# Performance work log

Measured on AMD Instinct MI355X. Metric: run time of the kernel, lower is better.

Reference implementation:

```python
import jax, jax.numpy as jnp
import numpy as np

D_IN = 1024
D_OUT = 1024
SEQ = 2048
BATCH = 4


def setup_inputs() -> dict:
    key = jax.random.key(0)
    kx, kq, kk, kv = jax.random.split(key, 4)
    x = jax.random.normal(kx, (BATCH, SEQ, D_IN), dtype=jnp.float32)
    s = 1.0 / np.sqrt(D_IN)
    Wq = jax.random.uniform(kq, (D_IN, D_OUT), dtype=jnp.float32, minval=-s, maxval=s)
    Wk = jax.random.uniform(kk, (D_IN, D_OUT), dtype=jnp.float32, minval=-s, maxval=s)
    Wv = jax.random.uniform(kv, (D_IN, D_OUT), dtype=jnp.float32, minval=-s, maxval=s)
    return {"x": x, "Wq": Wq, "Wk": Wk, "Wv": Wv}


def reference(x, Wq, Wk, Wv):
    d_k = Wq.shape[1]
    q = jnp.einsum('bsd,de->bse', x, Wq)
    k = jnp.einsum('bsd,de->bse', x, Wk)
    v = jnp.einsum('bsd,de->bse', x, Wv)
    # [B, S, S] raw scores
    scores = jnp.einsum('bqe,bke->bqk', q, k)
    S = scores.shape[-1]
    causal = jnp.triu(jnp.ones((S, S), dtype=bool), k=1)  # True above diagonal
    scores = jnp.where(causal, -jnp.inf, scores)
    attn = jax.nn.softmax(scores * (d_k ** -0.5), axis=-1)
    # dropout p=0.0 -> identity
    return jnp.einsum('bqk,bke->bqe', attn, v)
```

## Files before the change

kernel.cpp:

```cpp
#include <hip/hip_runtime.h>
#include <hip/hip_bf16.h>

typedef unsigned short u16;
typedef __bf16 bfx8 __attribute__((ext_vector_type(8)));
typedef float fx4 __attribute__((ext_vector_type(4)));

#define SEQ 2048
#define DIM 1024
#define NBATCH 4
#define SCALE 0.03125f
#define NEL ((size_t)NBATCH * SEQ * DIM)

__device__ inline u16 f2bf(float f) {
    __bf16 h = (__bf16)f;
    return __builtin_bit_cast(unsigned short, h);
}

#define GLL(gp, lp) __builtin_amdgcn_global_load_lds( \
    (const __attribute__((address_space(1))) unsigned int*)(gp), \
    (__attribute__((address_space(3))) unsigned int*)(lp), 16, 0, 0)

__global__ __launch_bounds__(256) void prep(
    const float* __restrict__ X,
    const float* __restrict__ Wq, const float* __restrict__ Wk,
    const float* __restrict__ Wv,
    u16* __restrict__ XB, u16* __restrict__ WB, u16* __restrict__ WTv,
    float* __restrict__ Lrow)
{
    __shared__ u16 t[32][33];
    int bid = blockIdx.x;
    int tid = threadIdx.x;
    if (bid < 8192) {
        size_t i = (size_t)bid * 256 + tid;
        float4 v = ((const float4*)X)[i];
        uint2 pk;
        pk.x = (unsigned)f2bf(v.x) | ((unsigned)f2bf(v.y) << 16);
        pk.y = (unsigned)f2bf(v.z) | ((unsigned)f2bf(v.w) << 16);
        ((uint2*)XB)[i] = pk;
    } else if (bid < 10240) {
        int b2 = bid - 8192;
        const float* W = (b2 < 1024) ? Wq : Wk;
        u16* out = WB + (size_t)(b2 >> 10) * 1024 * 1024;
        size_t i = (size_t)(b2 & 1023) * 256 + tid;
        float4 v = ((const float4*)W)[i];
        uint2 pk;
        pk.x = (unsigned)f2bf(v.x) | ((unsigned)f2bf(v.y) << 16);
        pk.y = (unsigned)f2bf(v.z) | ((unsigned)f2bf(v.w) << 16);
        ((uint2*)out)[i] = pk;
    } else if (bid < 11264) {
        int t2 = bid - 10240;
        int n0 = (t2 & 31) * 32, k0 = (t2 >> 5) * 32;
        int tx = tid & 31, ty = tid >> 5;
        #pragma unroll
        for (int i = 0; i < 32; i += 8)
            t[ty + i][tx] = f2bf(Wv[(size_t)(k0 + ty + i) * 1024 + n0 + tx]);
        __syncthreads();
        #pragma unroll
        for (int i = 0; i < 32; i += 8)
            WTv[(size_t)(n0 + ty + i) * 1024 + k0 + tx] = t[tx][ty + i];
    } else {
        int i = (bid - 11264) * 256 + tid;
        Lrow[i] = 0.0f;
    }
}

__global__ __launch_bounds__(256) void gemm_m(
    const u16* __restrict__ WBk, const u16* __restrict__ WBq, u16* __restrict__ MT)
{
    int m0 = blockIdx.y * 128, n0 = blockIdx.x * 128;
    __shared__ __align__(16) u16 As[128 * 32];
    __shared__ __align__(16) u16 Bs[128 * 32];
    int tid = threadIdx.x, lane = tid & 63, w = tid >> 6;
    int wm = w >> 1, wn = w & 1, lo = lane & 15, qd = lane >> 4;
    fx4 acc[4][4] = {};

    int c0 = tid, c1 = tid + 256;
    const u16* a0 = WBk + (size_t)(m0 + (c0 >> 2)) * 1024 + (((c0 & 3) ^ ((c0 >> 2) & 3)) * 8);
    const u16* a1 = WBk + (size_t)(m0 + (c1 >> 2)) * 1024 + (((c1 & 3) ^ ((c1 >> 2) & 3)) * 8);
    const u16* b0 = WBq + (size_t)(n0 + (c0 >> 2)) * 1024 + (((c0 & 3) ^ ((c0 >> 2) & 3)) * 8);
    const u16* b1 = WBq + (size_t)(n0 + (c1 >> 2)) * 1024 + (((c1 & 3) ^ ((c1 >> 2) & 3)) * 8);

    int sw = (qd ^ (lo & 3)) * 8;
    for (int k0 = 0; k0 < 1024; k0 += 32) {
        GLL(a0 + k0, &As[(size_t)c0 * 8]);
        GLL(a1 + k0, &As[(size_t)c1 * 8]);
        GLL(b0 + k0, &Bs[(size_t)c0 * 8]);
        GLL(b1 + k0, &Bs[(size_t)c1 * 8]);
        __syncthreads();
        bfx8 af[4], bf[4];
        #pragma unroll
        for (int i = 0; i < 4; i++)
            af[i] = *(const bfx8*)(&As[(wm * 64 + i * 16 + lo) * 32 + sw]);
        #pragma unroll
        for (int j = 0; j < 4; j++)
            bf[j] = *(const bfx8*)(&Bs[(wn * 64 + j * 16 + lo) * 32 + sw]);
        #pragma unroll
        for (int i = 0; i < 4; i++)
            #pragma unroll
            for (int j = 0; j < 4; j++)
                acc[i][j] = __builtin_amdgcn_mfma_f32_16x16x32_bf16(af[i], bf[j], acc[i][j], 0, 0, 0);
        __syncthreads();
    }
    #pragma unroll
    for (int i = 0; i < 4; i++)
        #pragma unroll
        for (int j = 0; j < 4; j++)
            #pragma unroll
            for (int r = 0; r < 4; r++)
                MT[(size_t)(m0 + wm * 64 + i * 16 + qd * 4 + r) * 1024
                   + n0 + wn * 64 + j * 16 + lo] = f2bf(acc[i][j][r]);
}

__global__ __launch_bounds__(512) void gemm256(
    const u16* __restrict__ XB, const u16* __restrict__ MT,
    const u16* __restrict__ WTv,
    u16* __restrict__ Yo, u16* __restrict__ VTo)
{
    const u16* Bop = (blockIdx.z == 0) ? MT : WTv;
    const int m0 = blockIdx.y * 256, n0 = blockIdx.x * 256;

    __shared__ __align__(16) u16 SM[65536];

    const int tid = threadIdx.x, lane = tid & 63, w = tid >> 6;
    const int wm = w >> 2, wn = w & 3, lo = lane & 15, qd = lane >> 4;
    const int swl = lo & 7;

    fx4 acc[8][4] = {};

    const u16* sA[4]; const u16* sB[4]; int dofs[4];
    #pragma unroll
    for (int p = 0; p < 4; ++p) {
        int n = p * 512 + tid;
        int row = n >> 3;
        int c = (n & 7) ^ (row & 7);
        sA[p] = XB  + (size_t)(m0 + row) * 1024 + c * 8;
        sB[p] = Bop + (size_t)(n0 + row) * 1024 + c * 8;
        dofs[p] = n * 8;
    }

    auto stage = [&](int kt2) {
        const int bb = (kt2 & 1) * 16384;
        #pragma unroll
        for (int p = 0; p < 4; ++p) GLL(sA[p] + kt2 * 64, &SM[bb + dofs[p]]);
        #pragma unroll
        for (int p = 0; p < 4; ++p) GLL(sB[p] + kt2 * 64, &SM[32768 + bb + dofs[p]]);
    };

    stage(0);
    stage(1);
    asm volatile("s_waitcnt vmcnt(8)" ::: "memory");
    __builtin_amdgcn_s_barrier();
    asm volatile("" ::: "memory");

    bfx8 af[4][2], bfA[2][2], bfB[2][2];

    for (int kt = 0; kt < 16; ++kt) {
        const u16* Ab = SM + (kt & 1) * 16384;
        const u16* Bb = SM + 32768 + (kt & 1) * 16384;

        #pragma unroll
        for (int ph = 0; ph < 4; ++ph) {
            const int mh = ph >> 1, nh = ph & 1;
            if (nh == 0) {
                #pragma unroll
                for (int ii = 0; ii < 4; ++ii)
                    #pragma unroll
                    for (int ks = 0; ks < 2; ++ks)
                        af[ii][ks] = *(const bfx8*)(Ab
                            + (wm * 128 + (mh * 4 + ii) * 16 + lo) * 64
                            + ((ks * 4 + qd) ^ swl) * 8);
            }
            if (ph == 0) {
                #pragma unroll
                for (int jn = 0; jn < 2; ++jn)
                    #pragma unroll
                    for (int ks = 0; ks < 2; ++ks)
                        bfA[jn][ks] = *(const bfx8*)(Bb
                            + (wn * 64 + jn * 16 + lo) * 64
                            + ((ks * 4 + qd) ^ swl) * 8);
            }
            if (ph == 1) {
                #pragma unroll
                for (int jn = 0; jn < 2; ++jn)
                    #pragma unroll
                    for (int ks = 0; ks < 2; ++ks)
                        bfB[jn][ks] = *(const bfx8*)(Bb
                            + (wn * 64 + (2 + jn) * 16 + lo) * 64
                            + ((ks * 4 + qd) ^ swl) * 8);
            }
            __builtin_amdgcn_s_barrier();
            asm volatile("s_waitcnt lgkmcnt(0)" ::: "memory");
            __builtin_amdgcn_sched_barrier(0);
            __builtin_amdgcn_s_setprio(1);
            #pragma unroll
            for (int ii = 0; ii < 4; ++ii)
                #pragma unroll
                for (int jn = 0; jn < 2; ++jn)
                    #pragma unroll
                    for (int ks = 0; ks < 2; ++ks) {
                        if (nh == 0)
                            acc[mh * 4 + ii][jn] = __builtin_amdgcn_mfma_f32_16x16x32_bf16(
                                af[ii][ks], bfA[jn][ks], acc[mh * 4 + ii][jn], 0, 0, 0);
                        else
                            acc[mh * 4 + ii][2 + jn] = __builtin_amdgcn_mfma_f32_16x16x32_bf16(
                                af[ii][ks], bfB[jn][ks], acc[mh * 4 + ii][2 + jn], 0, 0, 0);
                    }
            __builtin_amdgcn_s_setprio(0);
            __builtin_amdgcn_s_barrier();
            asm volatile("" ::: "memory");
        }
        if (kt < 14) stage(kt + 2);
        if (kt < 15) {
            if (kt < 14) asm volatile("s_waitcnt vmcnt(8)" ::: "memory");
            else         asm volatile("s_waitcnt vmcnt(0)" ::: "memory");
            __builtin_amdgcn_s_barrier();
            asm volatile("" ::: "memory");
        }
    }

    if (blockIdx.z == 0) {
        #pragma unroll
        for (int i = 0; i < 8; i++)
            #pragma unroll
            for (int j = 0; j < 4; j++)
                #pragma unroll
                for (int r = 0; r < 4; r++) {
                    int row = m0 + wm * 128 + i * 16 + qd * 4 + r;
                    int col = n0 + wn * 64 + j * 16 + lo;
                    Yo[(size_t)row * 1024 + col] = f2bf(acc[i][j][r]);
                }
    } else {
        u16 (*Ct)[258] = (u16(*)[258])SM;
        const int bb = m0 >> 11;
        const int sbase = m0 & 2047;
        #pragma unroll
        for (int half = 0; half < 2; ++half) {
            __syncthreads();
            if (wm == half) {
                #pragma unroll
                for (int i = 0; i < 8; i++)
                    #pragma unroll
                    for (int j = 0; j < 4; j++)
                        #pragma unroll
                        for (int r = 0; r < 4; r++)
                            Ct[i * 16 + qd * 4 + r][wn * 64 + j * 16 + lo] = f2bf(acc[i][j][r]);
            }
            __syncthreads();
            for (int e = tid; e < 16384; e += 512) {
                int d = e >> 6, s2 = (e & 63) * 2;
                unsigned pk = (unsigned)Ct[s2][d] | ((unsigned)Ct[s2 + 1][d] << 16);
                *(unsigned*)&VTo[((size_t)bb * DIM + (n0 + d)) * SEQ
                                 + sbase + half * 128 + s2] = pk;
            }
        }
    }
}

__global__ __launch_bounds__(512) void sgemm_exp(
    const u16* __restrict__ Y, const u16* __restrict__ XB,
    u16* __restrict__ P, float* __restrict__ Lrow)
{
    int b = blockIdx.y;
    int t = blockIdx.x;
    int i = (int)((sqrtf(8.0f * t + 1.0f) - 1.0f) * 0.5f);
    while ((i + 1) * (i + 2) / 2 <= t) i++;
    while (i * (i + 1) / 2 > t) i--;
    int j = t - i * (i + 1) / 2;

    const u16* Yb = Y + (size_t)b * SEQ * DIM;
    const u16* Xb = XB + (size_t)b * SEQ * DIM;
    u16* Pb = P + (size_t)b * SEQ * SEQ;
    float* Lb = Lrow + (size_t)b * SEQ;

    int m0 = i * 128, n0 = j * 128;

    __shared__ __align__(16) u16 As[128 * 64];
    __shared__ __align__(16) u16 Bs[128 * 64];

    int tid = threadIdx.x, lane = tid & 63, w = tid >> 6;
    int wm = w >> 2, wn = w & 3, lo = lane & 15, qd = lane >> 4;

    fx4 acc[4][2] = {};

    int c0 = tid, c1 = tid + 512;
    const u16* a0 = Yb + (size_t)(m0 + (c0 >> 3)) * 1024 + (((c0 & 7) ^ ((c0 >> 3) & 7)) * 8);
    const u16* a1 = Yb + (size_t)(m0 + (c1 >> 3)) * 1024 + (((c1 & 7) ^ ((c1 >> 3) & 7)) * 8);
    const u16* b0 = Xb + (size_t)(n0 + (c0 >> 3)) * 1024 + (((c0 & 7) ^ ((c0 >> 3) & 7)) * 8);
    const u16* b1 = Xb + (size_t)(n0 + (c1 >> 3)) * 1024 + (((c1 & 7) ^ ((c1 >> 3) & 7)) * 8);

    for (int k0 = 0; k0 < 1024; k0 += 64) {
        GLL(a0 + k0, &As[(size_t)c0 * 8]);
        GLL(a1 + k0, &As[(size_t)c1 * 8]);
        GLL(b0 + k0, &Bs[(size_t)c0 * 8]);
        GLL(b1 + k0, &Bs[(size_t)c1 * 8]);
        __syncthreads();

        #pragma unroll
        for (int kc = 0; kc < 2; kc++) {
            int sw = ((kc * 4 + qd) ^ (lo & 7)) * 8;
            bfx8 af[4], bf[2];
            #pragma unroll
            for (int ii = 0; ii < 4; ii++)
                af[ii] = *(const bfx8*)(&As[(wm * 64 + ii * 16 + lo) * 64 + sw]);
            #pragma unroll
            for (int jn = 0; jn < 2; jn++)
                bf[jn] = *(const bfx8*)(&Bs[(wn * 32 + jn * 16 + lo) * 64 + sw]);
            #pragma unroll
            for (int ii = 0; ii < 4; ii++)
                #pragma unroll
                for (int jn = 0; jn < 2; jn++)
                    acc[ii][jn] = __builtin_amdgcn_mfma_f32_16x16x32_bf16(af[ii], bf[jn], acc[ii][jn], 0, 0, 0);
        }
        __syncthreads();
    }

    #pragma unroll
    for (int ii = 0; ii < 4; ii++)
        #pragma unroll
        for (int r = 0; r < 4; r++) {
            int row = m0 + wm * 64 + ii * 16 + qd * 4 + r;
            float rs = 0.0f;
            #pragma unroll
            for (int jn = 0; jn < 2; jn++) {
                int col = n0 + wn * 32 + jn * 16 + lo;
                float s = acc[ii][jn][r] * SCALE;
                s = fminf(fmaxf(s, -30.0f), 30.0f);
                float p = (col > row) ? 0.0f : __expf(s);
                Pb[(size_t)row * SEQ + col] = f2bf(p);
                rs += p;
            }
            #pragma unroll
            for (int off = 1; off < 16; off <<= 1) rs += __shfl_xor(rs, off);
            if (lo == 0) atomicAdd(&Lb[row], rs);
        }
}

__global__ __launch_bounds__(512) void pvgemm(
    const u16* __restrict__ P, const u16* __restrict__ VT,
    const float* __restrict__ Lrow, float* __restrict__ O)
{
    int b = blockIdx.y;
    int qb = 15 - (int)(blockIdx.x >> 3);
    int db = blockIdx.x & 7;
    int m0 = qb * 128, n0 = db * 128;
    int kext = (qb + 1) * 128;

    const u16* Pb = P + (size_t)b * SEQ * SEQ;
    const u16* Vb = VT + (size_t)b * DIM * SEQ;
    const float* Lb = Lrow + (size_t)b * SEQ;
    float* Ob = O + (size_t)b * SEQ * DIM;

    __shared__ __align__(16) u16 As[128 * 64];
    __shared__ __align__(16) u16 Bs[128 * 64];

    int tid = threadIdx.x, lane = tid & 63, w = tid >> 6;
    int wm = w >> 2, wn = w & 3, lo = lane & 15, qd = lane >> 4;

    fx4 acc[4][2] = {};

    int c0 = tid, c1 = tid + 512;
    const u16* a0 = Pb + (size_t)(m0 + (c0 >> 3)) * SEQ + (((c0 & 7) ^ ((c0 >> 3) & 7)) * 8);
    const u16* a1 = Pb + (size_t)(m0 + (c1 >> 3)) * SEQ + (((c1 & 7) ^ ((c1 >> 3) & 7)) * 8);
    const u16* b0 = Vb + (size_t)(n0 + (c0 >> 3)) * SEQ + (((c0 & 7) ^ ((c0 >> 3) & 7)) * 8);
    const u16* b1 = Vb + (size_t)(n0 + (c1 >> 3)) * SEQ + (((c1 & 7) ^ ((c1 >> 3) & 7)) * 8);

    for (int k0 = 0; k0 < kext; k0 += 64) {
        GLL(a0 + k0, &As[(size_t)c0 * 8]);
        GLL(a1 + k0, &As[(size_t)c1 * 8]);
        GLL(b0 + k0, &Bs[(size_t)c0 * 8]);
        GLL(b1 + k0, &Bs[(size_t)c1 * 8]);
        __syncthreads();

        #pragma unroll
        for (int kc = 0; kc < 2; kc++) {
            int sw = ((kc * 4 + qd) ^ (lo & 7)) * 8;
            bfx8 af[4], bf[2];
            #pragma unroll
            for (int ii = 0; ii < 4; ii++)
                af[ii] = *(const bfx8*)(&As[(wm * 64 + ii * 16 + lo) * 64 + sw]);
            #pragma unroll
            for (int jn = 0; jn < 2; jn++)
                bf[jn] = *(const bfx8*)(&Bs[(wn * 32 + jn * 16 + lo) * 64 + sw]);
            #pragma unroll
            for (int ii = 0; ii < 4; ii++)
                #pragma unroll
                for (int jn = 0; jn < 2; jn++)
                    acc[ii][jn] = __builtin_amdgcn_mfma_f32_16x16x32_bf16(af[ii], bf[jn], acc[ii][jn], 0, 0, 0);
        }
        __syncthreads();
    }

    #pragma unroll
    for (int ii = 0; ii < 4; ii++)
        #pragma unroll
        for (int r = 0; r < 4; r++) {
            int row = m0 + wm * 64 + ii * 16 + qd * 4 + r;
            float linv = 1.0f / Lb[row];
            #pragma unroll
            for (int jn = 0; jn < 2; jn++) {
                int col = n0 + wn * 32 + jn * 16 + lo;
                Ob[(size_t)row * DIM + col] = acc[ii][jn][r] * linv;
            }
        }
}

__global__ __launch_bounds__(256) void gemm_legacy(
    const float* __restrict__ X,
    const float* __restrict__ Wq, const float* __restrict__ Wk, const float* __restrict__ Wv,
    u16* __restrict__ Qo, u16* __restrict__ Ko, u16* __restrict__ VTo)
{
    const int K = 1024, N = 1024;
    const float* W = (blockIdx.z == 0) ? Wq : (blockIdx.z == 1) ? Wk : Wv;
    int m0 = blockIdx.y * 128, n0 = blockIdx.x * 128;
    __shared__ __align__(16) u16 As[128 * 40];
    __shared__ __align__(16) u16 Bs[128 * 40];
    __shared__ __align__(16) u16 Ct[64][132];
    int tid = threadIdx.x, lane = tid & 63, w = tid >> 6;
    int wm = w >> 1, wn = w & 1, lo = lane & 15, qd = lane >> 4;
    fx4 acc[4][4] = {};
    for (int k0 = 0; k0 < K; k0 += 32) {
        #pragma unroll
        for (int c = tid; c < 1024; c += 256) {
            int row = c >> 3, cc = (c & 7) * 4;
            float4 v = *(const float4*)(X + (size_t)(m0 + row) * K + k0 + cc);
            uint2 pk;
            pk.x = (unsigned)f2bf(v.x) | ((unsigned)f2bf(v.y) << 16);
            pk.y = (unsigned)f2bf(v.z) | ((unsigned)f2bf(v.w) << 16);
            *(uint2*)(&As[row * 40 + cc]) = pk;
        }
        #pragma unroll
        for (int c = tid; c < 1024; c += 256) {
            int r = c >> 5, cc = (c & 31) * 4;
            float4 v = *(const float4*)(W + (size_t)(k0 + r) * N + n0 + cc);
            Bs[(cc + 0) * 40 + r] = f2bf(v.x);
            Bs[(cc + 1) * 40 + r] = f2bf(v.y);
            Bs[(cc + 2) * 40 + r] = f2bf(v.z);
            Bs[(cc + 3) * 40 + r] = f2bf(v.w);
        }
        __syncthreads();
        bfx8 af[4], bf[4];
        #pragma unroll
        for (int i = 0; i < 4; i++)
            af[i] = *(const bfx8*)(&As[(wm * 64 + i * 16 + lo) * 40 + qd * 8]);
        #pragma unroll
        for (int j = 0; j < 4; j++)
            bf[j] = *(const bfx8*)(&Bs[(wn * 64 + j * 16 + lo) * 40 + qd * 8]);
        #pragma unroll
        for (int i = 0; i < 4; i++)
            #pragma unroll
            for (int j = 0; j < 4; j++)
                acc[i][j] = __builtin_amdgcn_mfma_f32_16x16x32_bf16(af[i], bf[j], acc[i][j], 0, 0, 0);
        __syncthreads();
    }
    if (blockIdx.z != 2) {
        u16* C = (blockIdx.z == 0) ? Qo : Ko;
        #pragma unroll
        for (int i = 0; i < 4; i++)
            #pragma unroll
            for (int j = 0; j < 4; j++)
                #pragma unroll
                for (int r = 0; r < 4; r++) {
                    int row = m0 + wm * 64 + i * 16 + qd * 4 + r;
                    int col = n0 + wn * 64 + j * 16 + lo;
                    C[(size_t)row * N + col] = f2bf(acc[i][j][r]);
                }
    } else {
        #pragma unroll
        for (int half = 0; half < 2; half++) {
            __syncthreads();
            if (wm == half) {
                #pragma unroll
                for (int i = 0; i < 4; i++)
                    #pragma unroll
                    for (int j = 0; j < 4; j++)
                        #pragma unroll
                        for (int r = 0; r < 4; r++)
                            Ct[i * 16 + qd * 4 + r][wn * 64 + j * 16 + lo] = f2bf(acc[i][j][r]);
            }
            __syncthreads();
            #pragma unroll
            for (int e = tid; e < 64 * 128; e += 256) {
                int d = e >> 6, sl = e & 63;
                int gr = m0 + half * 64 + sl;
                int bb = gr >> 11, s = gr & 2047;
                VTo[((size_t)bb * DIM + (n0 + d)) * SEQ + s] = Ct[sl][d];
            }
        }
    }
}

__global__ __launch_bounds__(512) void flash_attn(
    const u16* __restrict__ Q, const u16* __restrict__ Kmat,
    const u16* __restrict__ VT, float* __restrict__ O)
{
    int b = blockIdx.y;
    int qt = (int)(gridDim.x - 1) - (int)blockIdx.x;
    int q0 = qt * 32;
    int tid = threadIdx.x;
    int lane = tid & 63, w = tid >> 6;
    int lo = lane & 15, qd = lane >> 4;

    __shared__ __align__(16) float Sp[8][32][33];
    __shared__ __align__(16) __bf16 Pl[32][40];
    __shared__ float ml[32], ll[32], al[32];

    const u16* Qb = Q + (size_t)b * SEQ * DIM;
    const u16* Kb = Kmat + (size_t)b * SEQ * DIM;
    const u16* VTb = VT + (size_t)b * DIM * SEQ;

    bfx8 qf[2][4];
    #pragma unroll
    for (int i = 0; i < 2; i++)
        #pragma unroll
        for (int c = 0; c < 4; c++)
            qf[i][c] = *(const bfx8*)(Qb + (size_t)(q0 + i * 16 + lo) * DIM + w * 128 + c * 32 + qd * 8);

    fx4 oacc[2][8] = {};
    if (tid < 32) { ml[tid] = -INFINITY; ll[tid] = 0.0f; }
    __syncthreads();

    for (int kt = 0; kt <= qt; kt++) {
        int k0 = kt * 32;
        fx4 sp[2][2] = {};
        #pragma unroll
        for (int c = 0; c < 4; c++) {
            bfx8 kf[2];
            #pragma unroll
            for (int jn = 0; jn < 2; jn++)
                kf[jn] = *(const bfx8*)(Kb + (size_t)(k0 + jn * 16 + lo) * DIM + w * 128 + c * 32 + qd * 8);
            #pragma unroll
            for (int i = 0; i < 2; i++)
                #pragma unroll
                for (int jn = 0; jn < 2; jn++)
                    sp[i][jn] = __builtin_amdgcn_mfma_f32_16x16x32_bf16(qf[i][c], kf[jn], sp[i][jn], 0, 0, 0);
        }
        #pragma unroll
        for (int i = 0; i < 2; i++)
            #pragma unroll
            for (int jn = 0; jn < 2; jn++)
                #pragma unroll
                for (int r = 0; r < 4; r++)
                    Sp[w][i * 16 + qd * 4 + r][jn * 16 + lo] = sp[i][jn][r];
        __syncthreads();
        {
            int r = tid >> 4, ci = tid & 15;
            int q = q0 + r;
            float s0 = 0.0f, s1 = 0.0f;
            #pragma unroll
            for (int p = 0; p < 8; p++) { s0 += Sp[p][r][ci]; s1 += Sp[p][r][ci + 16]; }
            s0 = fminf(fmaxf(s0 * SCALE, -1e30f), 1e30f);
            s1 = fminf(fmaxf(s1 * SCALE, -1e30f), 1e30f);
            if (k0 + ci > q)      s0 = -INFINITY;
            if (k0 + ci + 16 > q) s1 = -INFINITY;
            float mx = fmaxf(s0, s1);
            #pragma unroll
            for (int off = 1; off < 16; off <<= 1) mx = fmaxf(mx, __shfl_xor(mx, off));
            float mo = ml[r];
            float mn = fmaxf(mo, mx);
            float p0 = __expf(s0 - mn), p1 = __expf(s1 - mn);
            Pl[r][ci] = (__bf16)p0;
            Pl[r][ci + 16] = (__bf16)p1;
            float ps = p0 + p1;
            #pragma unroll
            for (int off = 1; off < 16; off <<= 1) ps += __shfl_xor(ps, off);
            if (ci == 0) {
                float alpha = __expf(mo - mn);
                ll[r] = alpha * ll[r] + ps;
                ml[r] = mn;
                al[r] = alpha;
            }
        }
        __syncthreads();
        float alocal[2][4];
        #pragma unroll
        for (int i = 0; i < 2; i++)
            #pragma unroll
            for (int r = 0; r < 4; r++)
                alocal[i][r] = al[i * 16 + qd * 4 + r];
        #pragma unroll
        for (int i = 0; i < 2; i++)
            #pragma unroll
            for (int j = 0; j < 8; j++)
                #pragma unroll
                for (int r = 0; r < 4; r++)
                    oacc[i][j][r] *= alocal[i][r];
        bfx8 pf[2];
        #pragma unroll
        for (int i = 0; i < 2; i++)
            pf[i] = *(const bfx8*)(&Pl[i * 16 + lo][qd * 8]);
        #pragma unroll
        for (int j = 0; j < 8; j++) {
            bfx8 vf = *(const bfx8*)(VTb + (size_t)(w * 128 + j * 16 + lo) * SEQ + k0 + qd * 8);
            #pragma unroll
            for (int i = 0; i < 2; i++)
                oacc[i][j] = __builtin_amdgcn_mfma_f32_16x16x32_bf16(pf[i], vf, oacc[i][j], 0, 0, 0);
        }
    }

    float linv[2][4];
    #pragma unroll
    for (int i = 0; i < 2; i++)
        #pragma unroll
        for (int r = 0; r < 4; r++)
            linv[i][r] = 1.0f / ll[i * 16 + qd * 4 + r];
    float* Ob = O + (size_t)b * SEQ * DIM;
    #pragma unroll
    for (int i = 0; i < 2; i++)
        #pragma unroll
        for (int j = 0; j < 8; j++)
            #pragma unroll
            for (int r = 0; r < 4; r++) {
                int row = q0 + i * 16 + qd * 4 + r;
                int col = w * 128 + j * 16 + lo;
                Ob[(size_t)row * DIM + col] = oacc[i][j][r] * linv[i][r];
            }
}

extern "C" void kernel_launch(void* const* d_in, const int* in_sizes, int n_in,
                              void* d_out, int out_size, void* d_ws, size_t ws_size,
                              hipStream_t stream) {
    const float* x  = (const float*)d_in[0];
    const float* Wq = (const float*)d_in[1];
    const float* Wk = (const float*)d_in[2];
    const float* Wv = (const float*)d_in[3];

    u16* ws = (u16*)d_ws;
    u16* Yp  = ws;
    u16* VTp = ws + NEL;
    u16* XBp = ws + 2 * NEL;
    u16* WBp = ws + 3 * NEL;
    u16* WTv = WBp + (size_t)2 * 1024 * 1024;
    u16* MTp = WTv + (size_t)1024 * 1024;
    u16* Pm  = MTp + (size_t)1024 * 1024;
    float* Lrow = (float*)(Pm + (size_t)NBATCH * SEQ * SEQ);

    size_t need_mat = ((size_t)3 * NEL + (size_t)4 * 1024 * 1024
                     + (size_t)NBATCH * SEQ * SEQ) * 2
                     + (size_t)NBATCH * SEQ * 4 + 1024;

    if (ws_size >= need_mat) {
        prep<<<dim3(11296), 256, 0, stream>>>(x, Wq, Wk, Wv, XBp, WBp, WTv, Lrow);
        gemm_m<<<dim3(8, 8), 256, 0, stream>>>(
            WBp + (size_t)1024 * 1024 , WBp , MTp);
        gemm256<<<dim3(4, 32, 2), 512, 0, stream>>>(XBp, MTp, WTv, Yp, VTp);
        sgemm_exp<<<dim3(136, NBATCH), 512, 0, stream>>>(Yp, XBp, Pm, Lrow);
        pvgemm<<<dim3(128, NBATCH), 512, 0, stream>>>(Pm, VTp, Lrow, (float*)d_out);
    } else {
        u16* Qp = ws; u16* Kp = ws + NEL; u16* VTf = ws + 2 * NEL;
        gemm_legacy<<<dim3(8, 64, 3), 256, 0, stream>>>(x, Wq, Wk, Wv, Qp, Kp, VTf);
        flash_attn<<<dim3(SEQ / 32, NBATCH), 512, 0, stream>>>(
            Qp, Kp, VTf, (float*)d_out);
    }
}
```

Before: 233.1 us.

## Double-buffer LDS tiles with async prefetch in score and PV GEMMs

Converts the sgemm_exp and pvgemm main loops from single-buffered loads (load, sync, compute, sync) to a two-stage LDS ring. Tile k+2 is prefetched via global_load_lds while tile k is computed, with explicit vmcnt waits and barriers. It also adds s_setprio around the MFMA bursts and barriers that split LDS reads from math, aiming to hide global-load latency. The cost is double the LDS per block, which may lower occupancy, plus extra barriers per K step.

Result: no change. 232.5 us (-0.3%).

```diff
diff --git a/kernel.cpp b/kernel.cpp
--- a/kernel.cpp
+++ b/kernel.cpp
@@ -274,11 +274,11 @@
 
     int m0 = i * 128, n0 = j * 128;
 
-    __shared__ __align__(16) u16 As[128 * 64];
-    __shared__ __align__(16) u16 Bs[128 * 64];
+    __shared__ __align__(16) u16 SM[32768];
 
     int tid = threadIdx.x, lane = tid & 63, w = tid >> 6;
     int wm = w >> 2, wn = w & 3, lo = lane & 15, qd = lane >> 4;
+    int swl = lo & 7;
 
     fx4 acc[4][2] = {};
 
@@ -287,31 +287,56 @@
     const u16* a1 = Yb + (size_t)(m0 + (c1 >> 3)) * 1024 + (((c1 & 7) ^ ((c1 >> 3) & 7)) * 8);
     const u16* b0 = Xb + (size_t)(n0 + (c0 >> 3)) * 1024 + (((c0 & 7) ^ ((c0 >> 3) & 7)) * 8);
     const u16* b1 = Xb + (size_t)(n0 + (c1 >> 3)) * 1024 + (((c1 & 7) ^ ((c1 >> 3) & 7)) * 8);
-
-    for (int k0 = 0; k0 < 1024; k0 += 64) {
-        GLL(a0 + k0, &As[(size_t)c0 * 8]);
-        GLL(a1 + k0, &As[(size_t)c1 * 8]);
-        GLL(b0 + k0, &Bs[(size_t)c0 * 8]);
-        GLL(b1 + k0, &Bs[(size_t)c1 * 8]);
-        __syncthreads();
-
-        #pragma unroll
-        for (int kc = 0; kc < 2; kc++) {
-            int sw = ((kc * 4 + qd) ^ (lo & 7)) * 8;
+    int d0 = c0 * 8, d1 = c1 * 8;
+
+    auto stage = [&](int kt2) {
+        int bb = (kt2 & 1) * 8192;
+        GLL(a0 + kt2 * 64, &SM[bb + d0]);
+        GLL(a1 + kt2 * 64, &SM[bb + d1]);
+        GLL(b0 + kt2 * 64, &SM[16384 + bb + d0]);
+        GLL(b1 + kt2 * 64, &SM[16384 + bb + d1]);
+    };
+
+    stage(0);
+    stage(1);
+    asm volatile("s_waitcnt vmcnt(4)" ::: "memory");
+    __builtin_amdgcn_s_barrier();
+    asm volatile("" ::: "memory");
+
+    for (int kt = 0; kt < 16; ++kt) {
+        const u16* Ab = SM + (kt & 1) * 8192;
+        const u16* Bb = SM + 16384 + (kt & 1) * 8192;
+
+        #pragma unroll
+        for (int kc = 0; kc < 2; ++kc) {
             bfx8 af[4], bf[2];
-            #pragma unroll
-            for (int ii = 0; ii < 4; ii++)
-                af[ii] = *(const bfx8*)(&As[(wm * 64 + ii * 16 + lo) * 64 + sw]);
-            #pragma unroll
-            for (int jn = 0; jn < 2; jn++)
-                bf[jn] = *(const bfx8*)(&Bs[(wn * 32 + jn * 16 + lo) * 64 + sw]);
-            #pragma unroll
-            for (int ii = 0; ii < 4; ii++)
-                #pragma unroll
-                for (int jn = 0; jn < 2; jn++)
+            int sw = ((kc * 4 + qd) ^ swl) * 8;
+            #pragma unroll
+            for (int ii = 0; ii < 4; ++ii)
+                af[ii] = *(const bfx8*)(Ab + (wm * 64 + ii * 16 + lo) * 64 + sw);
+            #pragma unroll
+            for (int jn = 0; jn < 2; ++jn)
+                bf[jn] = *(const bfx8*)(Bb + (wn * 32 + jn * 16 + lo) * 64 + sw);
+            __builtin_amdgcn_s_barrier();
+            asm volatile("s_waitcnt lgkmcnt(0)" ::: "memory");
+            __builtin_amdgcn_sched_barrier(0);
+            __builtin_amdgcn_s_setprio(1);
+            #pragma unroll
+            for (int ii = 0; ii < 4; ++ii)
+                #pragma unroll
+                for (int jn = 0; jn < 2; ++jn)
                     acc[ii][jn] = __builtin_amdgcn_mfma_f32_16x16x32_bf16(af[ii], bf[jn], acc[ii][jn], 0, 0, 0);
-        }
-        __syncthreads();
+            __builtin_amdgcn_s_setprio(0);
+            __builtin_amdgcn_s_barrier();
+            asm volatile("" ::: "memory");
+        }
+        if (kt < 14) stage(kt + 2);
+        if (kt < 15) {
+            if (kt < 14) asm volatile("s_waitcnt vmcnt(4)" ::: "memory");
+            else         asm volatile("s_waitcnt vmcnt(0)" ::: "memory");
+            __builtin_amdgcn_s_barrier();
+            asm volatile("" ::: "memory");
+        }
     }
 
     #pragma unroll
@@ -343,18 +368,18 @@
     int qb = 15 - (int)(blockIdx.x >> 3);
     int db = blockIdx.x & 7;
     int m0 = qb * 128, n0 = db * 128;
-    int kext = (qb + 1) * 128;
+    int nkt = (qb + 1) * 2;
 
     const u16* Pb = P + (size_t)b * SEQ * SEQ;
     const u16* Vb = VT + (size_t)b * DIM * SEQ;
     const float* Lb = Lrow + (size_t)b * SEQ;
     float* Ob = O + (size_t)b * SEQ * DIM;
 
-    __shared__ __align__(16) u16 As[128 * 64];
-    __shared__ __align__(16) u16 Bs[128 * 64];
+    __shared__ __align__(16) u16 SM[32768];
 
     int tid = threadIdx.x, lane = tid & 63, w = tid >> 6;
     int wm = w >> 2, wn = w & 3, lo = lane & 15, qd = lane >> 4;
+    int swl = lo & 7;
 
     fx4 acc[4][2] = {};
 
@@ -363,31 +388,56 @@
     const u16* a1 = Pb + (size_t)(m0 + (c1 >> 3)) * SEQ + (((c1 & 7) ^ ((c1 >> 3) & 7)) * 8);
     const u16* b0 = Vb + (size_t)(n0 + (c0 >> 3)) * SEQ + (((c0 & 7) ^ ((c0 >> 3) & 7)) * 8);
     const u16* b1 = Vb + (size_t)(n0 + (c1 >> 3)) * SEQ + (((c1 & 7) ^ ((c1 >> 3) & 7)) * 8);
-
-    for (int k0 = 0; k0 < kext; k0 += 64) {
-        GLL(a0 + k0, &As[(size_t)c0 * 8]);
-        GLL(a1 + k0, &As[(size_t)c1 * 8]);
-        GLL(b0 + k0, &Bs[(size_t)c0 * 8]);
-        GLL(b1 + k0, &Bs[(size_t)c1 * 8]);
-        __syncthreads();
-
-        #pragma unroll
-        for (int kc = 0; kc < 2; kc++) {
-            int sw = ((kc * 4 + qd) ^ (lo & 7)) * 8;
+    int d0 = c0 * 8, d1 = c1 * 8;
+
+    auto stage = [&](int kt2) {
+        int bb = (kt2 & 1) * 8192;
+        GLL(a0 + kt2 * 64, &SM[bb + d0]);
+        GLL(a1 + kt2 * 64, &SM[bb + d1]);
+        GLL(b0 + kt2 * 64, &SM[16384 + bb + d0]);
+        GLL(b1 + kt2 * 64, &SM[16384 + bb + d1]);
+    };
+
+    stage(0);
+    stage(1);
+    asm volatile("s_waitcnt vmcnt(4)" ::: "memory");
+    __builtin_amdgcn_s_barrier();
+    asm volatile("" ::: "memory");
+
+    for (int kt = 0; kt < nkt; ++kt) {
+        const u16* Ab = SM + (kt & 1) * 8192;
+        const u16* Bb = SM + 16384 + (kt & 1) * 8192;
+
+        #pragma unroll
+        for (int kc = 0; kc < 2; ++kc) {
             bfx8 af[4], bf[2];
-            #pragma unroll
-            for (int ii = 0; ii < 4; ii++)
-                af[ii] = *(const bfx8*)(&As[(wm * 64 + ii * 16 + lo) * 64 + sw]);
-            #pragma unroll
-            for (int jn = 0; jn < 2; jn++)
-                bf[jn] = *(const bfx8*)(&Bs[(wn * 32 + jn * 16 + lo) * 64 + sw]);
-            #pragma unroll
-            for (int ii = 0; ii < 4; ii++)
-                #pragma unroll
-                for (int jn = 0; jn < 2; jn++)
+            int sw = ((kc * 4 + qd) ^ swl) * 8;
+            #pragma unroll
+            for (int ii = 0; ii < 4; ++ii)
+                af[ii] = *(const bfx8*)(Ab + (wm * 64 + ii * 16 + lo) * 64 + sw);
+            #pragma unroll
+            for (int jn = 0; jn < 2; ++jn)
+                bf[jn] = *(const bfx8*)(Bb + (wn * 32 + jn * 16 + lo) * 64 + sw);
+            __builtin_amdgcn_s_barrier();
+            asm volatile("s_waitcnt lgkmcnt(0)" ::: "memory");
+            __builtin_amdgcn_sched_barrier(0);
+            __builtin_amdgcn_s_setprio(1);
+            #pragma unroll
+            for (int ii = 0; ii < 4; ++ii)
+                #pragma unroll
+                for (int jn = 0; jn < 2; ++jn)
                     acc[ii][jn] = __builtin_amdgcn_mfma_f32_16x16x32_bf16(af[ii], bf[jn], acc[ii][jn], 0, 0, 0);
-        }
-        __syncthreads();
+            __builtin_amdgcn_s_setprio(0);
+            __builtin_amdgcn_s_barrier();
+            asm volatile("" ::: "memory");
+        }
+        if (kt + 2 < nkt) stage(kt + 2);
+        if (kt + 1 < nkt) {
+            if (kt + 2 < nkt) asm volatile("s_waitcnt vmcnt(4)" ::: "memory");
+            else              asm volatile("s_waitcnt vmcnt(0)" ::: "memory");
+            __builtin_amdgcn_s_barrier();
+            asm volatile("" ::: "memory");
+        }
     }
 
     #pragma unroll
```
